# Optimization experiments

Hardware: AMD Instinct MI355X
Metric: run time of the kernel (lower is better)

## Reference

```python
import jax, jax.numpy as jnp
import numpy as np

B, S, D = 1, 2048, 1024   # batch, seq_len, d_model
E, F, TOP_K = 8, 4096, 2  # num_experts, d_ff, top_k


def setup_inputs() -> dict:
    key = jax.random.key(0)
    k0, k1, k2, k3, k4 = jax.random.split(key, 5)
    s = 0.02
    x = jax.random.normal(k0, (B, S, D), jnp.float32)
    Wr = jax.random.normal(k1, (D, E), jnp.float32) * s          # router
    W1 = jax.random.normal(k2, (E, D, F), jnp.float32) * s       # gate proj per expert
    W3 = jax.random.normal(k3, (E, D, F), jnp.float32) * s       # up proj per expert
    W2 = jax.random.normal(k4, (E, F, D), jnp.float32) * s       # down proj per expert
    return {"x": x, "Wr": Wr, "W1": W1, "W2": W2, "W3": W3}


def reference(x, Wr, W1, W2, W3):
    b, s, d = x.shape
    e = Wr.shape[1]
    xt = x.reshape(b * s, d)                       # [T, D]
    logits = xt @ Wr                               # [T, E]
    top_v, top_i = jax.lax.top_k(logits, TOP_K)    # [T, K]
    probs = jax.nn.softmax(top_v, axis=-1)         # softmax over selected experts
    # combine[t, e] = prob of expert e for token t (0 if not selected)
    combine = jnp.sum(probs[..., None] * jax.nn.one_hot(top_i, e, dtype=xt.dtype), axis=1)  # [T, E]
    # SwiGLU FFN per expert (dense grouped-GEMM form of the gather/scatter loop)
    h = jnp.einsum('td,edf->etf', xt, W1)          # [E, T, F]
    g = jnp.einsum('td,edf->etf', xt, W3)          # [E, T, F]
    y = jnp.einsum('etf,efd->etd', jax.nn.silu(h) * g, W2)  # [E, T, D]
    out = jnp.einsum('etd,te->td', y, combine)     # weighted combine
    return out.reshape(b, s, d)
```

## Files before the change

### kernel.cpp

```cpp
#include <hip/hip_runtime.h>
#include <hip/hip_bf16.h>

#define T_TOK 2048
#define DDIM  1024
#define NEXP  8
#define FDIM  4096
#define ROWS  (4096 + 256)

typedef __attribute__((ext_vector_type(8))) short bf16x8;
typedef __attribute__((ext_vector_type(4))) float f32x4;

#define SBW(n) ((((n) >> 3) ^ (n)) & 7)

__device__ __forceinline__ unsigned short f2b(float f) {
  union { float f; unsigned u; } v; v.f = f;
  unsigned r = v.u + 0x7FFF + ((v.u >> 16) & 1);
  return (unsigned short)(r >> 16);
}
__device__ __forceinline__ float b2f(unsigned short s) {
  union { unsigned u; float f; } v; v.u = ((unsigned)s) << 16;
  return v.f;
}
__device__ __forceinline__ unsigned cvtpk(float lo, float hi) {
  unsigned r;
  asm("v_cvt_pk_bf16_f32 %0, %1, %2" : "=v"(r) : "v"(lo), "v"(hi));
  return r;
}
__device__ __forceinline__ void gl16(const unsigned short* g, unsigned short* l) {
  __builtin_amdgcn_global_load_lds(
      (const __attribute__((address_space(1))) unsigned int*)(const void*)g,
      (__attribute__((address_space(3))) unsigned int*)(void*)l, 16, 0, 0);
}
__device__ __forceinline__ bf16x8 pack8(const float4* br, int c) {
  union { bf16x8 v; unsigned u[4]; } p;
  p.u[0] = cvtpk((&br[0].x)[c], (&br[1].x)[c]);
  p.u[1] = cvtpk((&br[2].x)[c], (&br[3].x)[c]);
  p.u[2] = cvtpk((&br[4].x)[c], (&br[5].x)[c]);
  p.u[3] = cvtpk((&br[6].x)[c], (&br[7].x)[c]);
  return p.v;
}
#define BAR_VM12_LGKM0()                                          \
  __builtin_amdgcn_sched_barrier(0);                              \
  asm volatile("s_waitcnt vmcnt(12) lgkmcnt(0)" ::: "memory");    \
  __builtin_amdgcn_s_barrier();                                   \
  __builtin_amdgcn_sched_barrier(0)
#define BAR_PLAIN()                                               \
  __builtin_amdgcn_sched_barrier(0);                              \
  __builtin_amdgcn_s_barrier();                                   \
  __builtin_amdgcn_sched_barrier(0)

__global__ void router_kernel(const float* __restrict__ x, const float* __restrict__ Wr,
                              int* __restrict__ cnt, int* __restrict__ tok,
                              float* __restrict__ prb) {
  int t = (blockIdx.x * blockDim.x + threadIdx.x) >> 6;
  int lane = threadIdx.x & 63;
  if (t >= T_TOK) return;
  const float* xr = x + (size_t)t * DDIM;
  float acc[NEXP];
#pragma unroll
  for (int e = 0; e < NEXP; ++e) acc[e] = 0.f;
#pragma unroll
  for (int i = 0; i < 4; ++i) {
    int d0 = lane * 16 + i * 4;
    float4 xv = *reinterpret_cast<const float4*>(xr + d0);
#pragma unroll
    for (int j = 0; j < 4; ++j) {
      float xd = (&xv.x)[j];
      float4 w0 = *reinterpret_cast<const float4*>(Wr + (size_t)(d0 + j) * NEXP);
      float4 w1 = *reinterpret_cast<const float4*>(Wr + (size_t)(d0 + j) * NEXP + 4);
      acc[0] += xd * w0.x; acc[1] += xd * w0.y; acc[2] += xd * w0.z; acc[3] += xd * w0.w;
      acc[4] += xd * w1.x; acc[5] += xd * w1.y; acc[6] += xd * w1.z; acc[7] += xd * w1.w;
    }
  }
#pragma unroll
  for (int off = 32; off >= 1; off >>= 1)
#pragma unroll
    for (int e = 0; e < NEXP; ++e) acc[e] += __shfl_down(acc[e], off);
  if (lane == 0) {
    float v0 = -1e30f, v1 = -1e30f; int i0 = 0, i1 = 0;
#pragma unroll
    for (int e = 0; e < NEXP; ++e) {
      float v = acc[e];
      if (v > v0)      { v1 = v0; i1 = i0; v0 = v; i0 = e; }
      else if (v > v1) { v1 = v; i1 = e; }
    }
    float e1 = __expf(v1 - v0);
    float p0 = 1.f / (1.f + e1);
    float p1 = e1 * p0;
    int s0 = atomicAdd(&cnt[i0], 1);
    tok[i0 * T_TOK + s0] = t; prb[i0 * T_TOK + s0] = p0;
    int s1 = atomicAdd(&cnt[i1], 1);
    tok[i1 * T_TOK + s1] = t; prb[i1 * T_TOK + s1] = p1;
  }
}

__global__ void cvt_x_kernel(const float* __restrict__ in, unsigned short* __restrict__ o) {
  size_t i = ((size_t)blockIdx.x * 256 + threadIdx.x) * 8;
  float4 a = *reinterpret_cast<const float4*>(in + i);
  float4 b = *reinterpret_cast<const float4*>(in + i + 4);
  bf16x8 p;
  p[0] = (short)f2b(a.x); p[1] = (short)f2b(a.y); p[2] = (short)f2b(a.z); p[3] = (short)f2b(a.w);
  p[4] = (short)f2b(b.x); p[5] = (short)f2b(b.y); p[6] = (short)f2b(b.z); p[7] = (short)f2b(b.w);
  *reinterpret_cast<bf16x8*>(o + i) = p;
}

__global__ __launch_bounds__(256, 3)
void gemm1ab_kernel(const unsigned short* __restrict__ xb,
                    const float* __restrict__ W1, const float* __restrict__ W3,
                    const int* __restrict__ cnt, const int* __restrict__ tok,
                    unsigned short* __restrict__ act) {
  const int e = blockIdx.z;
  const int cn = cnt[e];
  const int r0 = blockIdx.y * 128;
  if (r0 >= cn) return;
  const int n0 = blockIdx.x * 64;
  int off = 0;
#pragma unroll
  for (int i = 0; i < NEXP; ++i) off += (i < e) ? cnt[i] : 0;

  __shared__ __align__(16) unsigned short sA[2][128 * 64];
  __shared__ __align__(16) unsigned short sB1[64 * 64];
  __shared__ __align__(16) unsigned short sB3[64 * 64];

  const int tid = threadIdx.x;
  const int lane = tid & 63;
  const int wid = tid >> 6;
  const int wm = wid >> 1, wn = wid & 1;

  const unsigned short* asrc[4];
#pragma unroll
  for (int i = 0; i < 4; ++i) {
    int row = (4 * wid + i) * 8 + (lane >> 3);
    int slot = r0 + row; if (slot >= cn) slot = cn - 1;
    int tk = tok[e * T_TOK + slot];
    int sl = (lane & 7) ^ (row & 7);
    asrc[i] = xb + (size_t)tk * DDIM + sl * 8;
  }

  const int lt = tid & 127;
  const int ko = lt >> 4;
  const int nc = (lt & 15) * 4;
  const float* bp = ((tid < 128) ? W1 : W3) + ((size_t)e * DDIM + 8 * ko) * FDIM + n0 + nc;
  unsigned short* wb = (tid < 128) ? sB1 : sB3;
  int woff[4];
#pragma unroll
  for (int c = 0; c < 4; ++c) woff[c] = (nc + c) * 64 + ((ko ^ SBW(nc + c)) * 8);

  float4 br[8];
#define LOADB1(K0)                                                              \
  _Pragma("unroll") for (int r = 0; r < 8; ++r)                                 \
      br[r] = *reinterpret_cast<const float4*>(bp + (size_t)((K0) + r) * FDIM);
#define WRITEB1()                                                               \
  _Pragma("unroll") for (int c = 0; c < 4; ++c)                                 \
      *reinterpret_cast<bf16x8*>(wb + woff[c]) = pack8(br, c);
#define STAGEA1(K0, BUF)                                                        \
  _Pragma("unroll") for (int i = 0; i < 4; ++i)                                 \
      gl16(asrc[i] + (K0), &sA[BUF][(4 * wid + i) * 512]);

  f32x4 ah[4][2], ag[4][2];
#pragma unroll
  for (int m = 0; m < 4; ++m)
#pragma unroll
    for (int n = 0; n < 2; ++n) { ah[m][n] = (f32x4){0,0,0,0}; ag[m][n] = (f32x4){0,0,0,0}; }

  LOADB1(0);
  STAGEA1(0, 0);

  int cur = 0;
  for (int k0 = 0; k0 < DDIM; k0 += 64, cur ^= 1) {
    WRITEB1();
    const int kn = (k0 + 64) & (DDIM - 1);
    LOADB1(kn);
    STAGEA1(kn, cur ^ 1);
    BAR_VM12_LGKM0();
    __builtin_amdgcn_s_setprio(1);
#pragma unroll
    for (int kk = 0; kk < 2; ++kk) {
      int kc8 = kk * 4 + (lane >> 4);
      bf16x8 a[4], b1[2], b3[2];
#pragma unroll
      for (int m = 0; m < 4; ++m) {
        int row = wm * 64 + m * 16 + (lane & 15);
        a[m] = *reinterpret_cast<const bf16x8*>(&sA[cur][row * 64 + ((kc8 ^ (row & 7)) * 8)]);
      }
#pragma unroll
      for (int n = 0; n < 2; ++n) {
        int rowb = wn * 32 + n * 16 + (lane & 15);
        int offb = rowb * 64 + ((kc8 ^ SBW(rowb)) * 8);
        b1[n] = *reinterpret_cast<const bf16x8*>(&sB1[offb]);
        b3[n] = *reinterpret_cast<const bf16x8*>(&sB3[offb]);
      }
#pragma unroll
      for (int m = 0; m < 4; ++m)
#pragma unroll
        for (int n = 0; n < 2; ++n) {
          ah[m][n] = __builtin_amdgcn_mfma_f32_16x16x32_bf16(a[m], b1[n], ah[m][n], 0, 0, 0);
          ag[m][n] = __builtin_amdgcn_mfma_f32_16x16x32_bf16(a[m], b3[n], ag[m][n], 0, 0, 0);
        }
    }
    __builtin_amdgcn_s_setprio(0);
    BAR_PLAIN();
  }
#pragma unroll
  for (int m = 0; m < 4; ++m)
#pragma unroll
    for (int j = 0; j < 4; ++j) {
      int rloc = wm * 64 + m * 16 + (lane >> 4) * 4 + j;
      int s = r0 + rloc;
      if (s < cn) {
        unsigned short* orow = act + (size_t)(off + s) * FDIM + n0 + wn * 32 + (lane & 15);
#pragma unroll
        for (int n = 0; n < 2; ++n) {
          float hv = ah[m][n][j];
          float gv = ag[m][n][j];
          float sg = hv / (1.f + __expf(-hv));
          orow[n * 16] = f2b(sg * gv);
        }
      }
    }
}

__global__ __launch_bounds__(256, 3)
void gemm2d_kernel(const unsigned short* __restrict__ act, const float* __restrict__ W2,
                   const int* __restrict__ cnt, const int* __restrict__ tok,
                   const float* __restrict__ prb, float* __restrict__ out) {
  const int e = blockIdx.z >> 2;
  const int sp = blockIdx.z & 3;
  const int cn = cnt[e];
  const int r0 = blockIdx.y * 128;
  if (r0 >= cn) return;
  const int n0 = blockIdx.x * 128;
  const int kbase = sp * (FDIM / 4);
  int off = 0;
#pragma unroll
  for (int i = 0; i < NEXP; ++i) off += (i < e) ? cnt[i] : 0;

  __shared__ __align__(16) unsigned short sA[2][128 * 64];
  __shared__ __align__(16) unsigned short sB[128 * 64];

  const int tid = threadIdx.x;
  const int lane = tid & 63;
  const int wid = tid >> 6;
  const int wm = wid >> 1, wn = wid & 1;

  const unsigned short* asrc[4];
#pragma unroll
  for (int i = 0; i < 4; ++i) {
    int row = (4 * wid + i) * 8 + (lane >> 3);
    int sl = (lane & 7) ^ (row & 7);
    asrc[i] = act + (size_t)(off + r0 + row) * FDIM + kbase + sl * 8;
  }

  const int ko = tid >> 5;
  const int nc = (tid & 31) * 4;
  const float* bp = W2 + ((size_t)e * FDIM + kbase + 8 * ko) * DDIM + n0 + nc;
  int woff[4];
#pragma unroll
  for (int c = 0; c < 4; ++c) woff[c] = (nc + c) * 64 + ((ko ^ SBW(nc + c)) * 8);

  float4 br[8];
#define LOADB2(K0)                                                              \
  _Pragma("unroll") for (int r = 0; r < 8; ++r)                                 \
      br[r] = *reinterpret_cast<const float4*>(bp + (size_t)((K0) + r) * DDIM);
#define WRITEB2()                                                               \
  _Pragma("unroll") for (int c = 0; c < 4; ++c)                                 \
      *reinterpret_cast<bf16x8*>(&sB[woff[c]]) = pack8(br, c);
#define STAGEA2(K0, BUF)                                                        \
  _Pragma("unroll") for (int i = 0; i < 4; ++i)                                 \
      gl16(asrc[i] + (K0), &sA[BUF][(4 * wid + i) * 512]);

  f32x4 acc[4][4];
#pragma unroll
  for (int m = 0; m < 4; ++m)
#pragma unroll
    for (int n = 0; n < 4; ++n) acc[m][n] = (f32x4){0,0,0,0};

  LOADB2(0);
  STAGEA2(0, 0);

  int cur = 0;
  for (int k0 = 0; k0 < FDIM / 4; k0 += 64, cur ^= 1) {
    WRITEB2();
    const int kn = (k0 + 64) & (FDIM / 4 - 1);
    LOADB2(kn);
    STAGEA2(kn, cur ^ 1);
    BAR_VM12_LGKM0();
    __builtin_amdgcn_s_setprio(1);
#pragma unroll
    for (int kk = 0; kk < 2; ++kk) {
      int kc8 = kk * 4 + (lane >> 4);
      bf16x8 a[4], b[4];
#pragma unroll
      for (int m = 0; m < 4; ++m) {
        int row = wm * 64 + m * 16 + (lane & 15);
        a[m] = *reinterpret_cast<const bf16x8*>(&sA[cur][row * 64 + ((kc8 ^ (row & 7)) * 8)]);
      }
#pragma unroll
      for (int n = 0; n < 4; ++n) {
        int col = wn * 64 + n * 16 + (lane & 15);
        b[n] = *reinterpret_cast<const bf16x8*>(&sB[col * 64 + ((kc8 ^ SBW(col)) * 8)]);
      }
#pragma unroll
      for (int m = 0; m < 4; ++m)
#pragma unroll
        for (int n = 0; n < 4; ++n)
          acc[m][n] = __builtin_amdgcn_mfma_f32_16x16x32_bf16(a[m], b[n], acc[m][n], 0, 0, 0);
    }
    __builtin_amdgcn_s_setprio(0);
    BAR_PLAIN();
  }
#pragma unroll
  for (int m = 0; m < 4; ++m)
#pragma unroll
    for (int j = 0; j < 4; ++j) {
      int rloc = wm * 64 + m * 16 + (lane >> 4) * 4 + j;
      int s = r0 + rloc;
      if (s < cn) {
        int tkn = tok[e * T_TOK + s];
        float p = prb[e * T_TOK + s];
        float* orow = out + (size_t)tkn * DDIM + n0 + wn * 64 + (lane & 15);
#pragma unroll
        for (int n = 0; n < 4; ++n) atomicAdd(&orow[n * 16], p * acc[m][n][j]);
      }
    }
}

extern "C" void kernel_launch(void* const* d_in, const int* in_sizes, int n_in,
                              void* d_out, int out_size, void* d_ws, size_t ws_size,
                              hipStream_t stream) {
  const float* x  = (const float*)d_in[0];
  const float* Wr = (const float*)d_in[1];
  const float* W1 = (const float*)d_in[2];
  const float* W2 = (const float*)d_in[3];
  const float* W3 = (const float*)d_in[4];
  float* out = (float*)d_out;

  char* ws = (char*)d_ws;
  int*   cnt = (int*)ws;
  int*   tok = (int*)(ws + 1024);
  float* prb = (float*)(ws + 1024 + 65536);
  unsigned short* xb  = (unsigned short*)(ws + 256 * 1024);
  unsigned short* act = xb + (size_t)T_TOK * DDIM;

  hipMemsetAsync(cnt, 0, NEXP * sizeof(int), stream);
  hipMemsetAsync(d_out, 0, (size_t)out_size * sizeof(float), stream);

  router_kernel<<<T_TOK / 4, 256, 0, stream>>>(x, Wr, cnt, tok, prb);
  cvt_x_kernel<<<(T_TOK * DDIM) / (256 * 8), 256, 0, stream>>>(x, xb);
  gemm1ab_kernel<<<dim3(FDIM / 64, 16, NEXP), 256, 0, stream>>>(xb, W1, W3, cnt, tok, act);
  gemm2d_kernel<<<dim3(DDIM / 128, 16, NEXP * 4), 256, 0, stream>>>(act, W2, cnt, tok, prb, out);
}
```

Measured before the change: 316.9 us.

## Double the M tile to 256 rows in both expert GEMMs

Both grouped GEMM kernels now process 256 token rows per block instead of 128. Each wave owns 64 rows and the full N width, and the grid's row dimension is halved. Every fp32 weight tile read from global memory and converted to bf16 now feeds twice as many rows, which cuts weight traffic and conversion work. In exchange the kernels use more registers and LDS, occupancy drops from 3 to 2 blocks per CU, there are fewer blocks in flight, and padded rows waste more work when an expert receives few tokens.

```diff
diff --git a/kernel.cpp b/kernel.cpp
--- a/kernel.cpp
+++ b/kernel.cpp
@@ -39,9 +39,9 @@
   p.u[3] = cvtpk((&br[6].x)[c], (&br[7].x)[c]);
   return p.v;
 }
-#define BAR_VM12_LGKM0()                                          \
+#define BAR_VM16_LGKM0()                                          \
   __builtin_amdgcn_sched_barrier(0);                              \
-  asm volatile("s_waitcnt vmcnt(12) lgkmcnt(0)" ::: "memory");    \
+  asm volatile("s_waitcnt vmcnt(16) lgkmcnt(0)" ::: "memory");    \
   __builtin_amdgcn_s_barrier();                                   \
   __builtin_amdgcn_sched_barrier(0)
 #define BAR_PLAIN()                                               \
@@ -104,47 +104,43 @@
   *reinterpret_cast<bf16x8*>(o + i) = p;
 }
 
-__global__ __launch_bounds__(256, 3)
+__global__ __launch_bounds__(256, 2)
 void gemm1ab_kernel(const unsigned short* __restrict__ xb,
                     const float* __restrict__ W1, const float* __restrict__ W3,
                     const int* __restrict__ cnt, const int* __restrict__ tok,
                     unsigned short* __restrict__ act) {
   const int e = blockIdx.z;
   const int cn = cnt[e];
-  const int r0 = blockIdx.y * 128;
+  const int r0 = blockIdx.y * 256;
   if (r0 >= cn) return;
   const int n0 = blockIdx.x * 64;
   int off = 0;
 #pragma unroll
   for (int i = 0; i < NEXP; ++i) off += (i < e) ? cnt[i] : 0;
 
-  __shared__ __align__(16) unsigned short sA[2][128 * 64];
-  __shared__ __align__(16) unsigned short sB1[64 * 64];
-  __shared__ __align__(16) unsigned short sB3[64 * 64];
+  __shared__ __align__(16) unsigned short sA[2][256 * 64];
+  __shared__ __align__(16) unsigned short sB[128 * 64];
 
   const int tid = threadIdx.x;
   const int lane = tid & 63;
   const int wid = tid >> 6;
-  const int wm = wid >> 1, wn = wid & 1;
-
-  const unsigned short* asrc[4];
-#pragma unroll
-  for (int i = 0; i < 4; ++i) {
-    int row = (4 * wid + i) * 8 + (lane >> 3);
+
+  const unsigned short* asrc[8];
+#pragma unroll
+  for (int i = 0; i < 8; ++i) {
+    int row = wid * 64 + i * 8 + (lane >> 3);
     int slot = r0 + row; if (slot >= cn) slot = cn - 1;
     int tk = tok[e * T_TOK + slot];
     int sl = (lane & 7) ^ (row & 7);
     asrc[i] = xb + (size_t)tk * DDIM + sl * 8;
   }
 
-  const int lt = tid & 127;
-  const int ko = lt >> 4;
-  const int nc = (lt & 15) * 4;
-  const float* bp = ((tid < 128) ? W1 : W3) + ((size_t)e * DDIM + 8 * ko) * FDIM + n0 + nc;
-  unsigned short* wb = (tid < 128) ? sB1 : sB3;
+  const int kq = tid >> 5;
+  const int nc = (tid & 31) * 4;
+  const float* bp = ((nc < 64) ? W1 : W3) + ((size_t)e * DDIM + 8 * kq) * FDIM + n0 + (nc & 63);
   int woff[4];
 #pragma unroll
-  for (int c = 0; c < 4; ++c) woff[c] = (nc + c) * 64 + ((ko ^ SBW(nc + c)) * 8);
+  for (int c = 0; c < 4; ++c) woff[c] = (nc + c) * 64 + ((kq ^ SBW(nc + c)) * 8);
 
   float4 br[8];
 #define LOADB1(K0)                                                              \
@@ -152,16 +148,16 @@
       br[r] = *reinterpret_cast<const float4*>(bp + (size_t)((K0) + r) * FDIM);
 #define WRITEB1()                                                               \
   _Pragma("unroll") for (int c = 0; c < 4; ++c)                                 \
-      *reinterpret_cast<bf16x8*>(wb + woff[c]) = pack8(br, c);
+      *reinterpret_cast<bf16x8*>(&sB[woff[c]]) = pack8(br, c);
 #define STAGEA1(K0, BUF)                                                        \
-  _Pragma("unroll") for (int i = 0; i < 4; ++i)                                 \
-      gl16(asrc[i] + (K0), &sA[BUF][(4 * wid + i) * 512]);
-
-  f32x4 ah[4][2], ag[4][2];
+  _Pragma("unroll") for (int i = 0; i < 8; ++i)                                 \
+      gl16(asrc[i] + (K0), &sA[BUF][(wid * 8 + i) * 512]);
+
+  f32x4 ah[4][4], ag[4][4];
 #pragma unroll
   for (int m = 0; m < 4; ++m)
 #pragma unroll
-    for (int n = 0; n < 2; ++n) { ah[m][n] = (f32x4){0,0,0,0}; ag[m][n] = (f32x4){0,0,0,0}; }
+    for (int n = 0; n < 4; ++n) { ah[m][n] = (f32x4){0,0,0,0}; ag[m][n] = (f32x4){0,0,0,0}; }
 
   LOADB1(0);
   STAGEA1(0, 0);
@@ -172,28 +168,28 @@
     const int kn = (k0 + 64) & (DDIM - 1);
     LOADB1(kn);
     STAGEA1(kn, cur ^ 1);
-    BAR_VM12_LGKM0();
+    BAR_VM16_LGKM0();
     __builtin_amdgcn_s_setprio(1);
 #pragma unroll
     for (int kk = 0; kk < 2; ++kk) {
       int kc8 = kk * 4 + (lane >> 4);
-      bf16x8 a[4], b1[2], b3[2];
+      bf16x8 a[4], b1[4], b3[4];
 #pragma unroll
       for (int m = 0; m < 4; ++m) {
-        int row = wm * 64 + m * 16 + (lane & 15);
+        int row = wid * 64 + m * 16 + (lane & 15);
         a[m] = *reinterpret_cast<const bf16x8*>(&sA[cur][row * 64 + ((kc8 ^ (row & 7)) * 8)]);
       }
 #pragma unroll
-      for (int n = 0; n < 2; ++n) {
-        int rowb = wn * 32 + n * 16 + (lane & 15);
-        int offb = rowb * 64 + ((kc8 ^ SBW(rowb)) * 8);
-        b1[n] = *reinterpret_cast<const bf16x8*>(&sB1[offb]);
-        b3[n] = *reinterpret_cast<const bf16x8*>(&sB3[offb]);
+      for (int n = 0; n < 4; ++n) {
+        int v1r = n * 16 + (lane & 15);
+        b1[n] = *reinterpret_cast<const bf16x8*>(&sB[v1r * 64 + ((kc8 ^ SBW(v1r)) * 8)]);
+        int v3r = v1r + 64;
+        b3[n] = *reinterpret_cast<const bf16x8*>(&sB[v3r * 64 + ((kc8 ^ SBW(v3r)) * 8)]);
       }
 #pragma unroll
       for (int m = 0; m < 4; ++m)
 #pragma unroll
-        for (int n = 0; n < 2; ++n) {
+        for (int n = 0; n < 4; ++n) {
           ah[m][n] = __builtin_amdgcn_mfma_f32_16x16x32_bf16(a[m], b1[n], ah[m][n], 0, 0, 0);
           ag[m][n] = __builtin_amdgcn_mfma_f32_16x16x32_bf16(a[m], b3[n], ag[m][n], 0, 0, 0);
         }
@@ -205,12 +201,12 @@
   for (int m = 0; m < 4; ++m)
 #pragma unroll
     for (int j = 0; j < 4; ++j) {
-      int rloc = wm * 64 + m * 16 + (lane >> 4) * 4 + j;
+      int rloc = wid * 64 + m * 16 + (lane >> 4) * 4 + j;
       int s = r0 + rloc;
       if (s < cn) {
-        unsigned short* orow = act + (size_t)(off + s) * FDIM + n0 + wn * 32 + (lane & 15);
-#pragma unroll
-        for (int n = 0; n < 2; ++n) {
+        unsigned short* orow = act + (size_t)(off + s) * FDIM + n0 + (lane & 15);
+#pragma unroll
+        for (int n = 0; n < 4; ++n) {
           float hv = ah[m][n][j];
           float gv = ag[m][n][j];
           float sg = hv / (1.f + __expf(-hv));
@@ -220,14 +216,14 @@
     }
 }
 
-__global__ __launch_bounds__(256, 3)
+__global__ __launch_bounds__(256, 2)
 void gemm2d_kernel(const unsigned short* __restrict__ act, const float* __restrict__ W2,
                    const int* __restrict__ cnt, const int* __restrict__ tok,
                    const float* __restrict__ prb, float* __restrict__ out) {
   const int e = blockIdx.z >> 2;
   const int sp = blockIdx.z & 3;
   const int cn = cnt[e];
-  const int r0 = blockIdx.y * 128;
+  const int r0 = blockIdx.y * 256;
   if (r0 >= cn) return;
   const int n0 = blockIdx.x * 128;
   const int kbase = sp * (FDIM / 4);
@@ -235,28 +231,27 @@
 #pragma unroll
   for (int i = 0; i < NEXP; ++i) off += (i < e) ? cnt[i] : 0;
 
-  __shared__ __align__(16) unsigned short sA[2][128 * 64];
+  __shared__ __align__(16) unsigned short sA[2][256 * 64];
   __shared__ __align__(16) unsigned short sB[128 * 64];
 
   const int tid = threadIdx.x;
   const int lane = tid & 63;
   const int wid = tid >> 6;
-  const int wm = wid >> 1, wn = wid & 1;
-
-  const unsigned short* asrc[4];
-#pragma unroll
-  for (int i = 0; i < 4; ++i) {
-    int row = (4 * wid + i) * 8 + (lane >> 3);
+
+  const unsigned short* asrc[8];
+#pragma unroll
+  for (int i = 0; i < 8; ++i) {
+    int row = wid * 64 + i * 8 + (lane >> 3);
     int sl = (lane & 7) ^ (row & 7);
     asrc[i] = act + (size_t)(off + r0 + row) * FDIM + kbase + sl * 8;
   }
 
-  const int ko = tid >> 5;
+  const int kq = tid >> 5;
   const int nc = (tid & 31) * 4;
-  const float* bp = W2 + ((size_t)e * FDIM + kbase + 8 * ko) * DDIM + n0 + nc;
+  const float* bp = W2 + ((size_t)e * FDIM + kbase + 8 * kq) * DDIM + n0 + nc;
   int woff[4];
 #pragma unroll
-  for (int c = 0; c < 4; ++c) woff[c] = (nc + c) * 64 + ((ko ^ SBW(nc + c)) * 8);
+  for (int c = 0; c < 4; ++c) woff[c] = (nc + c) * 64 + ((kq ^ SBW(nc + c)) * 8);
 
   float4 br[8];
 #define LOADB2(K0)                                                              \
@@ -266,14 +261,14 @@
   _Pragma("unroll") for (int c = 0; c < 4; ++c)                                 \
       *reinterpret_cast<bf16x8*>(&sB[woff[c]]) = pack8(br, c);
 #define STAGEA2(K0, BUF)                                                        \
-  _Pragma("unroll") for (int i = 0; i < 4; ++i)                                 \
-      gl16(asrc[i] + (K0), &sA[BUF][(4 * wid + i) * 512]);
-
-  f32x4 acc[4][4];
+  _Pragma("unroll") for (int i = 0; i < 8; ++i)                                 \
+      gl16(asrc[i] + (K0), &sA[BUF][(wid * 8 + i) * 512]);
+
+  f32x4 acc[4][8];
 #pragma unroll
   for (int m = 0; m < 4; ++m)
 #pragma unroll
-    for (int n = 0; n < 4; ++n) acc[m][n] = (f32x4){0,0,0,0};
+    for (int n = 0; n < 8; ++n) acc[m][n] = (f32x4){0,0,0,0};
 
   LOADB2(0);
   STAGEA2(0, 0);
@@ -284,26 +279,26 @@
     const int kn = (k0 + 64) & (FDIM / 4 - 1);
     LOADB2(kn);
     STAGEA2(kn, cur ^ 1);
-    BAR_VM12_LGKM0();
+    BAR_VM16_LGKM0();
     __builtin_amdgcn_s_setprio(1);
 #pragma unroll
     for (int kk = 0; kk < 2; ++kk) {
       int kc8 = kk * 4 + (lane >> 4);
-      bf16x8 a[4], b[4];
+      bf16x8 a[4], b[8];
 #pragma unroll
       for (int m = 0; m < 4; ++m) {
-        int row = wm * 64 + m * 16 + (lane & 15);
+        int row = wid * 64 + m * 16 + (lane & 15);
         a[m] = *reinterpret_cast<const bf16x8*>(&sA[cur][row * 64 + ((kc8 ^ (row & 7)) * 8)]);
       }
 #pragma unroll
-      for (int n = 0; n < 4; ++n) {
-        int col = wn * 64 + n * 16 + (lane & 15);
+      for (int n = 0; n < 8; ++n) {
+        int col = n * 16 + (lane & 15);
         b[n] = *reinterpret_cast<const bf16x8*>(&sB[col * 64 + ((kc8 ^ SBW(col)) * 8)]);
       }
 #pragma unroll
       for (int m = 0; m < 4; ++m)
 #pragma unroll
-        for (int n = 0; n < 4; ++n)
+        for (int n = 0; n < 8; ++n)
           acc[m][n] = __builtin_amdgcn_mfma_f32_16x16x32_bf16(a[m], b[n], acc[m][n], 0, 0, 0);
     }
     __builtin_amdgcn_s_setprio(0);
@@ -313,14 +308,14 @@
   for (int m = 0; m < 4; ++m)
 #pragma unroll
     for (int j = 0; j < 4; ++j) {
-      int rloc = wm * 64 + m * 16 + (lane >> 4) * 4 + j;
+      int rloc = wid * 64 + m * 16 + (lane >> 4) * 4 + j;
       int s = r0 + rloc;
       if (s < cn) {
         int tkn = tok[e * T_TOK + s];
         float p = prb[e * T_TOK + s];
-        float* orow = out + (size_t)tkn * DDIM + n0 + wn * 64 + (lane & 15);
-#pragma unroll
-        for (int n = 0; n < 4; ++n) atomicAdd(&orow[n * 16], p * acc[m][n][j]);
+        float* orow = out + (size_t)tkn * DDIM + n0 + (lane & 15);
+#pragma unroll
+        for (int n = 0; n < 8; ++n) atomicAdd(&orow[n * 16], p * acc[m][n][j]);
       }
     }
 }
@@ -347,6 +342,6 @@
 
   router_kernel<<<T_TOK / 4, 256, 0, stream>>>(x, Wr, cnt, tok, prb);
   cvt_x_kernel<<<(T_TOK * DDIM) / (256 * 8), 256, 0, stream>>>(x, xb);
-  gemm1ab_kernel<<<dim3(FDIM / 64, 16, NEXP), 256, 0, stream>>>(xb, W1, W3, cnt, tok, act);
-  gemm2d_kernel<<<dim3(DDIM / 128, 16, NEXP * 4), 256, 0, stream>>>(act, W2, cnt, tok, prb, out);
-}
+  gemm1ab_kernel<<<dim3(FDIM / 64, 8, NEXP), 256, 0, stream>>>(xb, W1, W3, cnt, tok, act);
+  gemm2d_kernel<<<dim3(DDIM / 128, 8, NEXP * 4), 256, 0, stream>>>(act, W2, cnt, tok, prb, out);
+}
```

After: 323.7 us. 2.1% more time.

## Single-buffer A tiles and raise occupancy to four blocks per CU

Applied to the files above, without the earlier changes.

Both grouped GEMM kernels drop the double-buffered A shared-memory staging and the hand-tuned vmcnt barrier and setprio scheduling. Each k-step now uses plain __syncthreads: write B, stage A for the current step, sync, then prefetch the next B into registers. Launch bounds go from 3 to 4 blocks per CU, relying on the smaller LDS footprint and register budget. This trades explicit load/compute overlap within a block for more concurrent blocks to hide latency.

```diff
diff --git a/kernel.cpp b/kernel.cpp
--- a/kernel.cpp
+++ b/kernel.cpp
@@ -39,15 +39,6 @@
   p.u[3] = cvtpk((&br[6].x)[c], (&br[7].x)[c]);
   return p.v;
 }
-#define BAR_VM12_LGKM0()                                          \
-  __builtin_amdgcn_sched_barrier(0);                              \
-  asm volatile("s_waitcnt vmcnt(12) lgkmcnt(0)" ::: "memory");    \
-  __builtin_amdgcn_s_barrier();                                   \
-  __builtin_amdgcn_sched_barrier(0)
-#define BAR_PLAIN()                                               \
-  __builtin_amdgcn_sched_barrier(0);                              \
-  __builtin_amdgcn_s_barrier();                                   \
-  __builtin_amdgcn_sched_barrier(0)
 
 __global__ void router_kernel(const float* __restrict__ x, const float* __restrict__ Wr,
                               int* __restrict__ cnt, int* __restrict__ tok,
@@ -104,7 +95,7 @@
   *reinterpret_cast<bf16x8*>(o + i) = p;
 }
 
-__global__ __launch_bounds__(256, 3)
+__global__ __launch_bounds__(256, 4)
 void gemm1ab_kernel(const unsigned short* __restrict__ xb,
                     const float* __restrict__ W1, const float* __restrict__ W3,
                     const int* __restrict__ cnt, const int* __restrict__ tok,
@@ -118,7 +109,7 @@
 #pragma unroll
   for (int i = 0; i < NEXP; ++i) off += (i < e) ? cnt[i] : 0;
 
-  __shared__ __align__(16) unsigned short sA[2][128 * 64];
+  __shared__ __align__(16) unsigned short sA[128 * 64];
   __shared__ __align__(16) unsigned short sB1[64 * 64];
   __shared__ __align__(16) unsigned short sB3[64 * 64];
 
@@ -153,9 +144,9 @@
 #define WRITEB1()                                                               \
   _Pragma("unroll") for (int c = 0; c < 4; ++c)                                 \
       *reinterpret_cast<bf16x8*>(wb + woff[c]) = pack8(br, c);
-#define STAGEA1(K0, BUF)                                                        \
+#define STAGEA1(K0)                                                             \
   _Pragma("unroll") for (int i = 0; i < 4; ++i)                                 \
-      gl16(asrc[i] + (K0), &sA[BUF][(4 * wid + i) * 512]);
+      gl16(asrc[i] + (K0), &sA[(4 * wid + i) * 512]);
 
   f32x4 ah[4][2], ag[4][2];
 #pragma unroll
@@ -164,16 +155,13 @@
     for (int n = 0; n < 2; ++n) { ah[m][n] = (f32x4){0,0,0,0}; ag[m][n] = (f32x4){0,0,0,0}; }
 
   LOADB1(0);
-  STAGEA1(0, 0);
-
-  int cur = 0;
-  for (int k0 = 0; k0 < DDIM; k0 += 64, cur ^= 1) {
+
+  for (int k0 = 0; k0 < DDIM; k0 += 64) {
+    __syncthreads();
     WRITEB1();
-    const int kn = (k0 + 64) & (DDIM - 1);
-    LOADB1(kn);
-    STAGEA1(kn, cur ^ 1);
-    BAR_VM12_LGKM0();
-    __builtin_amdgcn_s_setprio(1);
+    STAGEA1(k0);
+    __syncthreads();
+    if (k0 + 64 < DDIM) LOADB1(k0 + 64);
 #pragma unroll
     for (int kk = 0; kk < 2; ++kk) {
       int kc8 = kk * 4 + (lane >> 4);
@@ -181,7 +169,7 @@
 #pragma unroll
       for (int m = 0; m < 4; ++m) {
         int row = wm * 64 + m * 16 + (lane & 15);
-        a[m] = *reinterpret_cast<const bf16x8*>(&sA[cur][row * 64 + ((kc8 ^ (row & 7)) * 8)]);
+        a[m] = *reinterpret_cast<const bf16x8*>(&sA[row * 64 + ((kc8 ^ (row & 7)) * 8)]);
       }
 #pragma unroll
       for (int n = 0; n < 2; ++n) {
@@ -198,8 +186,6 @@
           ag[m][n] = __builtin_amdgcn_mfma_f32_16x16x32_bf16(a[m], b3[n], ag[m][n], 0, 0, 0);
         }
     }
-    __builtin_amdgcn_s_setprio(0);
-    BAR_PLAIN();
   }
 #pragma unroll
   for (int m = 0; m < 4; ++m)
@@ -220,7 +206,7 @@
     }
 }
 
-__global__ __launch_bounds__(256, 3)
+__global__ __launch_bounds__(256, 4)
 void gemm2d_kernel(const unsigned short* __restrict__ act, const float* __restrict__ W2,
                    const int* __restrict__ cnt, const int* __restrict__ tok,
                    const float* __restrict__ prb, float* __restrict__ out) {
@@ -235,7 +221,7 @@
 #pragma unroll
   for (int i = 0; i < NEXP; ++i) off += (i < e) ? cnt[i] : 0;
 
-  __shared__ __align__(16) unsigned short sA[2][128 * 64];
+  __shared__ __align__(16) unsigned short sA[128 * 64];
   __shared__ __align__(16) unsigned short sB[128 * 64];
 
   const int tid = threadIdx.x;
@@ -265,9 +251,9 @@
 #define WRITEB2()                                                               \
   _Pragma("unroll") for (int c = 0; c < 4; ++c)                                 \
       *reinterpret_cast<bf16x8*>(&sB[woff[c]]) = pack8(br, c);
-#define STAGEA2(K0, BUF)                                                        \
+#define STAGEA2(K0)                                                             \
   _Pragma("unroll") for (int i = 0; i < 4; ++i)                                 \
-      gl16(asrc[i] + (K0), &sA[BUF][(4 * wid + i) * 512]);
+      gl16(asrc[i] + (K0), &sA[(4 * wid + i) * 512]);
 
   f32x4 acc[4][4];
 #pragma unroll
@@ -276,16 +262,13 @@
     for (int n = 0; n < 4; ++n) acc[m][n] = (f32x4){0,0,0,0};
 
   LOADB2(0);
-  STAGEA2(0, 0);
-
-  int cur = 0;
-  for (int k0 = 0; k0 < FDIM / 4; k0 += 64, cur ^= 1) {
+
+  for (int k0 = 0; k0 < FDIM / 4; k0 += 64) {
+    __syncthreads();
     WRITEB2();
-    const int kn = (k0 + 64) & (FDIM / 4 - 1);
-    LOADB2(kn);
-    STAGEA2(kn, cur ^ 1);
-    BAR_VM12_LGKM0();
-    __builtin_amdgcn_s_setprio(1);
+    STAGEA2(k0);
+    __syncthreads();
+    if (k0 + 64 < FDIM / 4) LOADB2(k0 + 64);
 #pragma unroll
     for (int kk = 0; kk < 2; ++kk) {
       int kc8 = kk * 4 + (lane >> 4);
@@ -293,7 +276,7 @@
 #pragma unroll
       for (int m = 0; m < 4; ++m) {
         int row = wm * 64 + m * 16 + (lane & 15);
-        a[m] = *reinterpret_cast<const bf16x8*>(&sA[cur][row * 64 + ((kc8 ^ (row & 7)) * 8)]);
+        a[m] = *reinterpret_cast<const bf16x8*>(&sA[row * 64 + ((kc8 ^ (row & 7)) * 8)]);
       }
 #pragma unroll
       for (int n = 0; n < 4; ++n) {
@@ -306,8 +289,6 @@
         for (int n = 0; n < 4; ++n)
           acc[m][n] = __builtin_amdgcn_mfma_f32_16x16x32_bf16(a[m], b[n], acc[m][n], 0, 0, 0);
     }
-    __builtin_amdgcn_s_setprio(0);
-    BAR_PLAIN();
   }
 #pragma unroll
   for (int m = 0; m < 4; ++m)
```

Result: slower. 611.4 us (+92.9%).
